# Kernel optimization log

Hardware: AMD Instinct MI355X
Metric: run time of the kernel (lower is better)

## Reference

```python
import jax, jax.numpy as jnp
import numpy as np

NEG_INF = 1e9  # matches module's -1000000000.0 masking constant


def setup_inputs() -> dict:
    key = jax.random.key(0)
    kq, kv = jax.random.split(key)
    B, T, D = 4, 2048, 1024
    query = jax.random.normal(kq, (B, T, D), dtype=jnp.float32)
    value = jax.random.normal(kv, (B, T, D), dtype=jnp.float32)
    return {"query": query, "value": value}


def reference(query, value):
    # key defaults to value (len(inputs) == 2 path)
    k = value
    # dot-product scores (canonical Keras Attention _calculate_scores)
    scores = jnp.einsum("bqd,bkd->bqk", query, k)  # [B, Tq, Tv]
    Tq, Tv = scores.shape[-2], scores.shape[-1]
    # causal lower-triangular mask over last two dims (row >= col)
    causal_mask = jnp.tril(jnp.ones((Tq, Tv), dtype=bool))  # [Tq, Tv]
    # scores -= 1e9 * (~mask), then softmax (eval mode: no dropout)
    scores = scores - NEG_INF * (~causal_mask).astype(scores.dtype)
    weights = jax.nn.softmax(scores, axis=-1)
    result = jnp.einsum("bqv,bvd->bqd", weights, value)
    return result
```

## Files before the change

kernel.cpp:

```cpp
#include <hip/hip_runtime.h>
#include <hip/hip_fp16.h>

typedef _Float16 half8 __attribute__((ext_vector_type(8)));
typedef float    floatx4 __attribute__((ext_vector_type(4)));
typedef unsigned int uintx4 __attribute__((ext_vector_type(4)));

#define MFMA16(a, b, c) __builtin_amdgcn_mfma_f32_16x16x32_f16((a), (b), (c), 0, 0, 0)

constexpr int T_ = 2048;
constexpr int D_ = 1024;
constexpr int NB = 4;
constexpr int NTILE = 136;
constexpr size_t PT_ELEMS = 16384;

__device__ __forceinline__ half8 cvt8(floatx4 a, floatx4 b) {
  half8 h;
  h[0] = (_Float16)a[0]; h[1] = (_Float16)a[1]; h[2] = (_Float16)a[2]; h[3] = (_Float16)a[3];
  h[4] = (_Float16)b[0]; h[5] = (_Float16)b[1]; h[6] = (_Float16)b[2]; h[7] = (_Float16)b[3];
  return h;
}

__device__ __forceinline__ void gl16(const void* g, void* l) {
  __builtin_amdgcn_global_load_lds(
      (const __attribute__((address_space(1))) void*)g,
      (__attribute__((address_space(3))) void*)l, 16, 0, 0);
}

__global__ __launch_bounds__(256) void cast_h(const float* __restrict__ X,
                                              _Float16* __restrict__ Xh) {
  const size_t i = ((size_t)blockIdx.x * 256 + threadIdx.x) * 8;
  *(half8*)(Xh + i) = cvt8(*(const floatx4*)(X + i), *(const floatx4*)(X + i + 4));
}

__global__ __launch_bounds__(256) void build_vt(const float* __restrict__ V,
                                                _Float16* __restrict__ VhT) {
  __shared__ _Float16 tile[64][65];
  const int bid = blockIdx.x;
  const int b = bid & 3, tt = (bid >> 2) & 31, dd = bid >> 7;
  const float* Vb = V + ((size_t)b * T_ + tt * 64) * D_ + dd * 64;
#pragma unroll
  for (int k = 0; k < 16; ++k) {
    const int e = k * 256 + threadIdx.x, r = e >> 6, c = e & 63;
    tile[r][c] = (_Float16)Vb[(size_t)r * D_ + c];
  }
  __syncthreads();
#pragma unroll
  for (int k = 0; k < 16; ++k) {
    const int e = k * 256 + threadIdx.x, dr = e >> 6, tc = e & 63;
    VhT[((size_t)b * D_ + dd * 64 + dr) * T_ + tt * 64 + tc] = tile[tc][dr];
  }
}

__global__ __launch_bounds__(256, 2) void sgemm(const _Float16* __restrict__ Qh,
                                                const _Float16* __restrict__ Vh,
                                                _Float16* __restrict__ Pt,
                                                float* __restrict__ mg,
                                                float* __restrict__ lg) {
  extern __shared__ __align__(16) char lds[];
  char* As = lds;
  char* Bs = lds + 32768;
  const int tid = threadIdx.x;
  const int w = tid >> 6, l = tid & 63, l15 = l & 15, hi = l >> 4;
  const int wr = (w >> 1) * 64, wc = (w & 1) * 64;

  const int b = (int)(blockIdx.x & 3);
  int rem = (int)(blockIdx.x >> 2), j = 0;
  while (rem >= 16 - j) { rem -= 16 - j; ++j; }
  const int i = j + rem;

  const _Float16* Qb = Qh + ((size_t)(b * T_ + i * 128)) * D_;
  const _Float16* Vb = Vh + ((size_t)(b * T_ + j * 128)) * D_;
  const int srow = w * 32 + (l >> 4);
  char* Adst = As + w * 8192;
  char* Bdst = Bs + w * 8192;

  floatx4 acc[4][4];
#pragma unroll
  for (int mi = 0; mi < 4; ++mi)
#pragma unroll
    for (int ni = 0; ni < 4; ++ni) acc[mi][ni] = (floatx4){0.f, 0.f, 0.f, 0.f};

  for (int s = 0; s < 8; ++s) {
#pragma unroll
    for (int q = 0; q < 8; ++q) {
      const int r0 = srow + q * 4;
      const int sc = ((l & 15) ^ (r0 & 15)) * 8;
      gl16(Qb + (size_t)r0 * D_ + s * 128 + sc, Adst + q * 1024);
      gl16(Vb + (size_t)r0 * D_ + s * 128 + sc, Bdst + q * 1024);
    }
    __syncthreads();
#pragma unroll
    for (int s32 = 0; s32 < 4; ++s32) {
      half8 af[4], bb[4];
#pragma unroll
      for (int mi = 0; mi < 4; ++mi) {
        const int row = wr + mi * 16 + l15;
        af[mi] = *(const half8*)(As + row * 256 + (((s32 * 4 + hi) ^ (row & 15)) << 4));
      }
#pragma unroll
      for (int ni = 0; ni < 4; ++ni) {
        const int row = wc + ni * 16 + l15;
        bb[ni] = *(const half8*)(Bs + row * 256 + (((s32 * 4 + hi) ^ (row & 15)) << 4));
      }
#pragma unroll
      for (int mi = 0; mi < 4; ++mi)
#pragma unroll
        for (int ni = 0; ni < 4; ++ni)
          acc[mi][ni] = MFMA16(af[mi], bb[ni], acc[mi][ni]);
    }
    __syncthreads();
  }

  float* Mex = (float*)Bs;
  float* Lex = (float*)(Bs + 1024);

  if (i == j) {
#pragma unroll
    for (int mi = 0; mi < 4; ++mi)
#pragma unroll
      for (int ni = 0; ni < 4; ++ni) {
        const int col = wc + ni * 16 + l15;
        const int row0 = wr + mi * 16 + 4 * hi;
#pragma unroll
        for (int r = 0; r < 4; ++r)
          if (col > row0 + r) acc[mi][ni][r] = -1e30f;
      }
  }

  floatx4 mrow[4];
#pragma unroll
  for (int mi = 0; mi < 4; ++mi) {
#pragma unroll
    for (int r = 0; r < 4; ++r)
      mrow[mi][r] = fmaxf(fmaxf(acc[mi][0][r], acc[mi][1][r]),
                          fmaxf(acc[mi][2][r], acc[mi][3][r]));
#pragma unroll
    for (int off = 1; off < 16; off <<= 1)
#pragma unroll
      for (int r = 0; r < 4; ++r)
        mrow[mi][r] = fmaxf(mrow[mi][r], __shfl_xor(mrow[mi][r], off));
  }
  if (l15 == 0) {
#pragma unroll
    for (int mi = 0; mi < 4; ++mi)
      *(floatx4*)&Mex[(w & 1) * 128 + wr + mi * 16 + 4 * hi] = mrow[mi];
  }
  __syncthreads();
#pragma unroll
  for (int mi = 0; mi < 4; ++mi) {
    const floatx4 m0 = *(const floatx4*)&Mex[wr + mi * 16 + 4 * hi];
    const floatx4 m1 = *(const floatx4*)&Mex[128 + wr + mi * 16 + 4 * hi];
#pragma unroll
    for (int r = 0; r < 4; ++r) mrow[mi][r] = fmaxf(m0[r], m1[r]);
  }

  floatx4 lsum[4];
#pragma unroll
  for (int mi = 0; mi < 4; ++mi) {
    lsum[mi] = (floatx4){0.f, 0.f, 0.f, 0.f};
    const int row0 = wr + mi * 16 + 4 * hi;
#pragma unroll
    for (int ni = 0; ni < 4; ++ni) {
      const int col = wc + ni * 16 + l15;
#pragma unroll
      for (int r = 0; r < 4; ++r) {
        const float p = __expf(acc[mi][ni][r] - mrow[mi][r]);
        lsum[mi][r] += p;
        *(_Float16*)(As + (row0 + r) * 256 + col * 2) = (_Float16)p;
      }
    }
#pragma unroll
    for (int off = 1; off < 16; off <<= 1)
#pragma unroll
      for (int r = 0; r < 4; ++r) lsum[mi][r] += __shfl_xor(lsum[mi][r], off);
  }
  if (l15 == 0) {
#pragma unroll
    for (int mi = 0; mi < 4; ++mi)
      *(floatx4*)&Lex[(w & 1) * 128 + wr + mi * 16 + 4 * hi] = lsum[mi];
  }
  __syncthreads();

  if (((w & 1) == 0) && l15 == 0) {
    const size_t base = ((size_t)(b * 16 + j)) * 2048 + i * 128;
#pragma unroll
    for (int mi = 0; mi < 4; ++mi) {
      const int r0 = wr + mi * 16 + 4 * hi;
      const floatx4 l0 = *(const floatx4*)&Lex[r0];
      const floatx4 l1 = *(const floatx4*)&Lex[128 + r0];
#pragma unroll
      for (int r = 0; r < 4; ++r) {
        mg[base + r0 + r] = mrow[mi][r];
        lg[base + r0 + r] = l0[r] + l1[r];
      }
    }
  }
  _Float16* Pg = Pt + (size_t)(b * NTILE + ((i * (i + 1)) >> 1) + j) * PT_ELEMS;
  const int drow = tid >> 1, dhalf = tid & 1;
#pragma unroll
  for (int k = 0; k < 8; ++k) {
    const int c = k ^ (tid & 7);
    const uintx4 v = *(const uintx4*)(As + drow * 256 + dhalf * 128 + c * 16);
    *(uintx4*)((char*)Pg + drow * 256 + dhalf * 128 + c * 16) = v;
  }
}

__global__ __launch_bounds__(256) void combine(const float* __restrict__ mg,
                                               const float* __restrict__ lg,
                                               _Float16* __restrict__ ah,
                                               float* __restrict__ linv) {
  const int gid = (int)(blockIdx.x * 256 + threadIdx.x);
  const int b = gid >> 11, row = gid & 2047, i = row >> 7;
  const size_t mb = (size_t)b * 32768 + row;
  float M = -1e30f;
  for (int j = 0; j <= i; ++j) M = fmaxf(M, mg[mb + (size_t)j * 2048]);
  float L = 0.f;
  for (int j = 0; j <= i; ++j) {
    const float a = __expf(mg[mb + (size_t)j * 2048] - M);
    L += a * lg[mb + (size_t)j * 2048];
    ah[((size_t)b * 2048 + row) * 16 + j] = (_Float16)a;
  }
  linv[b * 2048 + row] = 1.0f / L;
}

__global__ __launch_bounds__(256, 2) void pv(const _Float16* __restrict__ Pt,
                                             const _Float16* __restrict__ VhT,
                                             const _Float16* __restrict__ ah,
                                             const float* __restrict__ linv,
                                             float* __restrict__ O) {
  extern __shared__ __align__(16) char lds[];
  char* As = lds;
  char* Bs = lds + 32768;
  const int tid = threadIdx.x;
  const int w = tid >> 6, l = tid & 63, l15 = l & 15, hi = l >> 4;
  const int wr = (w >> 1) * 64, wc = (w & 1) * 64;

  const int b = (int)(blockIdx.x & 3), t = (int)(blockIdx.x >> 2);
  const int r_ = t >> 3;
  const int i = (r_ < 8) ? (15 - r_) : (r_ - 8);
  const int nc = t & 7;
  const int ns = i + 1;

  const _Float16* Pb = Pt + (size_t)(b * NTILE + ((i * (i + 1)) >> 1)) * PT_ELEMS;
  const _Float16* Vt = VhT + ((size_t)(b * D_ + nc * 128)) * T_;
  const int srow = w * 32 + (l >> 4);
  char* Adst = As + w * 8192;
  char* Bdst = Bs + w * 8192;

  floatx4 acc[4][4];
#pragma unroll
  for (int mi = 0; mi < 4; ++mi)
#pragma unroll
    for (int ni = 0; ni < 4; ++ni) acc[mi][ni] = (floatx4){0.f, 0.f, 0.f, 0.f};

  for (int s = 0; s < ns; ++s) {
    _Float16 aw[4];
#pragma unroll
    for (int mi = 0; mi < 4; ++mi)
      aw[mi] = ah[((size_t)(b * 2048 + i * 128 + wr + mi * 16 + l15)) * 16 + s];
#pragma unroll
    for (int q = 0; q < 8; ++q) {
      const int r0 = srow + q * 4;
      const int sc = ((l & 15) ^ (r0 & 15)) * 8;
      gl16(Pb + (size_t)s * PT_ELEMS + (size_t)r0 * 128 + sc, Adst + q * 1024);
      gl16(Vt + (size_t)r0 * T_ + s * 128 + sc, Bdst + q * 1024);
    }
    __syncthreads();
#pragma unroll
    for (int s32 = 0; s32 < 4; ++s32) {
      half8 af[4], bb[4];
#pragma unroll
      for (int mi = 0; mi < 4; ++mi) {
        const int row = wr + mi * 16 + l15;
        af[mi] = *(const half8*)(As + row * 256 + (((s32 * 4 + hi) ^ (row & 15)) << 4));
        af[mi] *= aw[mi];
      }
#pragma unroll
      for (int ni = 0; ni < 4; ++ni) {
        const int row = wc + ni * 16 + l15;
        bb[ni] = *(const half8*)(Bs + row * 256 + (((s32 * 4 + hi) ^ (row & 15)) << 4));
      }
#pragma unroll
      for (int mi = 0; mi < 4; ++mi)
#pragma unroll
        for (int ni = 0; ni < 4; ++ni)
          acc[mi][ni] = MFMA16(af[mi], bb[ni], acc[mi][ni]);
    }
    __syncthreads();
  }

  float* Ob = O + ((size_t)b * T_ + i * 128) * D_ + nc * 128;
#pragma unroll
  for (int mi = 0; mi < 4; ++mi)
#pragma unroll
    for (int r = 0; r < 4; ++r) {
      const int rl = wr + mi * 16 + 4 * hi + r;
      const float iv = linv[b * 2048 + i * 128 + rl];
#pragma unroll
      for (int ni = 0; ni < 4; ++ni)
        Ob[(size_t)rl * D_ + wc + ni * 16 + l15] = acc[mi][ni][r] * iv;
    }
}

__global__ __launch_bounds__(256) void attn_fb(const float* __restrict__ Q,
                                               const float* __restrict__ V,
                                               float* __restrict__ O) {
  __shared__ float sc[2048];
  __shared__ float red[4];
  const int b = (int)(blockIdx.x >> 11), m = (int)(blockIdx.x & 2047);
  const int tid = threadIdx.x;
  const float* Qr = Q + ((size_t)b * T_ + m) * D_;
  for (int kv = tid; kv <= m; kv += 256) {
    const float* Vr = V + ((size_t)b * T_ + kv) * D_;
    float s = 0.f;
    for (int d = 0; d < D_; d += 4) {
      floatx4 q4 = *(const floatx4*)(Qr + d), v4 = *(const floatx4*)(Vr + d);
      s += q4[0] * v4[0] + q4[1] * v4[1] + q4[2] * v4[2] + q4[3] * v4[3];
    }
    sc[kv] = s;
  }
  __syncthreads();
  float mx = -1e30f;
  for (int kv = tid; kv <= m; kv += 256) mx = fmaxf(mx, sc[kv]);
#pragma unroll
  for (int off = 1; off < 64; off <<= 1) mx = fmaxf(mx, __shfl_xor(mx, off));
  if ((tid & 63) == 0) red[tid >> 6] = mx;
  __syncthreads();
  mx = fmaxf(fmaxf(red[0], red[1]), fmaxf(red[2], red[3]));
  __syncthreads();
  float sum = 0.f;
  for (int kv = tid; kv <= m; kv += 256) { float p = __expf(sc[kv] - mx); sc[kv] = p; sum += p; }
#pragma unroll
  for (int off = 1; off < 64; off <<= 1) sum += __shfl_xor(sum, off);
  __syncthreads();
  if ((tid & 63) == 0) red[tid >> 6] = sum;
  __syncthreads();
  const float inv = 1.0f / (red[0] + red[1] + red[2] + red[3]);
  float* Or = O + ((size_t)b * T_ + m) * D_;
  const int d = tid * 4;
  floatx4 o = {0.f, 0.f, 0.f, 0.f};
  for (int kv = 0; kv <= m; ++kv) {
    const float p = sc[kv];
    const floatx4 v4 = *(const floatx4*)(V + ((size_t)b * T_ + kv) * D_ + d);
    o[0] += p * v4[0]; o[1] += p * v4[1]; o[2] += p * v4[2]; o[3] += p * v4[3];
  }
  o[0] *= inv; o[1] *= inv; o[2] *= inv; o[3] *= inv;
  *(floatx4*)(Or + d) = o;
}

extern "C" void kernel_launch(void* const* d_in, const int* in_sizes, int n_in,
                              void* d_out, int out_size, void* d_ws, size_t ws_size,
                              hipStream_t stream) {
  const float* q = (const float*)d_in[0];
  const float* v = (const float*)d_in[1];
  float* out = (float*)d_out;

  const size_t OFF_VH = 16777216;
  const size_t OFF_P  = 33554432;
  const size_t OFF_M  = OFF_P + (size_t)NB * NTILE * PT_ELEMS * 2;
  const size_t OFF_LT = OFF_M + 524288;
  const size_t OFF_AH = OFF_LT + 524288;
  const size_t OFF_LI = OFF_AH + 262144;
  const size_t NEED   = OFF_LI + 32768;

  if (ws_size >= NEED) {
    _Float16* qh = (_Float16*)d_ws;
    _Float16* vh = (_Float16*)((char*)d_ws + OFF_VH);
    _Float16* pt = (_Float16*)((char*)d_ws + OFF_P);
    float* mg = (float*)((char*)d_ws + OFF_M);
    float* lg = (float*)((char*)d_ws + OFF_LT);
    _Float16* ah = (_Float16*)((char*)d_ws + OFF_AH);
    float* li = (float*)((char*)d_ws + OFF_LI);
    hipFuncSetAttribute((const void*)sgemm, hipFuncAttributeMaxDynamicSharedMemorySize, 65536);
    hipFuncSetAttribute((const void*)pv, hipFuncAttributeMaxDynamicSharedMemorySize, 65536);
    cast_h<<<dim3(4096), dim3(256), 0, stream>>>(q, qh);
    cast_h<<<dim3(4096), dim3(256), 0, stream>>>(v, vh);
    sgemm<<<dim3(NB * NTILE), dim3(256), 65536, stream>>>(qh, vh, pt, mg, lg);
    combine<<<dim3(32), dim3(256), 0, stream>>>(mg, lg, ah, li);
    build_vt<<<dim3(2048), dim3(256), 0, stream>>>(v, qh);
    pv<<<dim3(512), dim3(256), 65536, stream>>>(pt, qh, ah, li, out);
  } else {
    attn_fb<<<dim3(NB * T_), dim3(256), 0, stream>>>(q, v, out);
  }
}
```

Baseline: 118.2 us.

## Restructure attention pipeline: fused prep, double-buffered 512-thread score and PV GEMMs

Merges the Q cast and V transpose into one prep kernel and drops the separate V fp16 cast: the score GEMM now reads fp32 V straight into LDS and converts it while loading fragments. Both GEMMs move to 512-thread blocks covering 256-row tiles, with double-buffered LDS staging (prefetch the next K slice before the MFMAs) and an explicit waitcnt/barrier sync. PV uses narrower 64-column output tiles, giving more blocks per CU, and zero-fills masked P tiles. This aims to cut launch count, global traffic and load stalls, at the cost of larger LDS use, fp32 B-tile bandwidth and wasted work on partially masked 256-row tiles.

```diff
diff --git a/kernel.cpp b/kernel.cpp
--- a/kernel.cpp
+++ b/kernel.cpp
@@ -11,7 +11,6 @@
 constexpr int D_ = 1024;
 constexpr int NB = 4;
 constexpr int NTILE = 136;
-constexpr size_t PT_ELEMS = 16384;
 
 __device__ __forceinline__ half8 cvt8(floatx4 a, floatx4 b) {
   half8 h;
@@ -26,17 +25,26 @@
       (__attribute__((address_space(3))) void*)l, 16, 0, 0);
 }
 
-__global__ __launch_bounds__(256) void cast_h(const float* __restrict__ X,
-                                              _Float16* __restrict__ Xh) {
-  const size_t i = ((size_t)blockIdx.x * 256 + threadIdx.x) * 8;
-  *(half8*)(Xh + i) = cvt8(*(const floatx4*)(X + i), *(const floatx4*)(X + i + 4));
-}
-
-__global__ __launch_bounds__(256) void build_vt(const float* __restrict__ V,
-                                                _Float16* __restrict__ VhT) {
+__device__ __forceinline__ void STEP_SYNC() {
+  asm volatile("s_waitcnt vmcnt(0) lgkmcnt(0)" ::: "memory");
+  __builtin_amdgcn_s_barrier();
+  __builtin_amdgcn_sched_barrier(0);
+}
+
+__global__ __launch_bounds__(256) void prep(const float* __restrict__ Q,
+                                            const float* __restrict__ V,
+                                            _Float16* __restrict__ Qh,
+                                            _Float16* __restrict__ VhT) {
   __shared__ _Float16 tile[64][65];
   const int bid = blockIdx.x;
-  const int b = bid & 3, tt = (bid >> 2) & 31, dd = bid >> 7;
+  if (bid < 2048) {
+    const size_t i = ((size_t)bid * 256 + threadIdx.x) * 16;
+    *(half8*)(Qh + i)     = cvt8(*(const floatx4*)(Q + i),     *(const floatx4*)(Q + i + 4));
+    *(half8*)(Qh + i + 8) = cvt8(*(const floatx4*)(Q + i + 8), *(const floatx4*)(Q + i + 12));
+    return;
+  }
+  const int b2 = bid - 2048;
+  const int b = b2 & 3, tt = (b2 >> 2) & 31, dd = b2 >> 7;
   const float* Vb = V + ((size_t)b * T_ + tt * 64) * D_ + dd * 64;
 #pragma unroll
   for (int k = 0; k < 16; ++k) {
@@ -51,28 +59,38 @@
   }
 }
 
-__global__ __launch_bounds__(256, 2) void sgemm(const _Float16* __restrict__ Qh,
-                                                const _Float16* __restrict__ Vh,
+__global__ __launch_bounds__(512, 2) void sgemm(const _Float16* __restrict__ Qh,
+                                                const float* __restrict__ V,
                                                 _Float16* __restrict__ Pt,
                                                 float* __restrict__ mg,
                                                 float* __restrict__ lg) {
   extern __shared__ __align__(16) char lds[];
-  char* As = lds;
-  char* Bs = lds + 32768;
   const int tid = threadIdx.x;
   const int w = tid >> 6, l = tid & 63, l15 = l & 15, hi = l >> 4;
   const int wr = (w >> 1) * 64, wc = (w & 1) * 64;
 
   const int b = (int)(blockIdx.x & 3);
   int rem = (int)(blockIdx.x >> 2), j = 0;
-  while (rem >= 16 - j) { rem -= 16 - j; ++j; }
-  const int i = j + rem;
-
-  const _Float16* Qb = Qh + ((size_t)(b * T_ + i * 128)) * D_;
-  const _Float16* Vb = Vh + ((size_t)(b * T_ + j * 128)) * D_;
-  const int srow = w * 32 + (l >> 4);
-  char* Adst = As + w * 8192;
-  char* Bdst = Bs + w * 8192;
+  while (rem >= 8 - (j >> 1)) { rem -= 8 - (j >> 1); ++j; }
+  const int I = (j >> 1) + rem;
+
+  const _Float16* Qb = Qh + ((size_t)(b * T_ + I * 256)) * D_;
+  const float*    Vb = V  + ((size_t)(b * T_ + j * 128)) * D_;
+
+  const int arow = w * 32 + (l >> 3);
+  const int brow = w * 16 + (l >> 4);
+
+  auto STAGE = [&](const int s, const int buf) {
+    char* Ad = lds + buf * 65536 + w * 4096;
+    char* Bd = lds + buf * 65536 + 32768 + w * 4096;
+#pragma unroll
+    for (int q = 0; q < 4; ++q) {
+      const int ar = arow + q * 8;
+      gl16(Qb + (size_t)ar * D_ + s * 64 + ((l & 7) ^ (ar & 7)) * 8, Ad + q * 1024);
+      const int br = brow + q * 4;
+      gl16(Vb + (size_t)br * D_ + s * 64 + ((l & 15) ^ (br & 15)) * 4, Bd + q * 1024);
+    }
+  };
 
   floatx4 acc[4][4];
 #pragma unroll
@@ -80,53 +98,66 @@
 #pragma unroll
     for (int ni = 0; ni < 4; ++ni) acc[mi][ni] = (floatx4){0.f, 0.f, 0.f, 0.f};
 
-  for (int s = 0; s < 8; ++s) {
-#pragma unroll
-    for (int q = 0; q < 8; ++q) {
-      const int r0 = srow + q * 4;
-      const int sc = ((l & 15) ^ (r0 & 15)) * 8;
-      gl16(Qb + (size_t)r0 * D_ + s * 128 + sc, Adst + q * 1024);
-      gl16(Vb + (size_t)r0 * D_ + s * 128 + sc, Bdst + q * 1024);
-    }
-    __syncthreads();
-#pragma unroll
-    for (int s32 = 0; s32 < 4; ++s32) {
-      half8 af[4], bb[4];
-#pragma unroll
-      for (int mi = 0; mi < 4; ++mi) {
-        const int row = wr + mi * 16 + l15;
-        af[mi] = *(const half8*)(As + row * 256 + (((s32 * 4 + hi) ^ (row & 15)) << 4));
-      }
-#pragma unroll
-      for (int ni = 0; ni < 4; ++ni) {
-        const int row = wc + ni * 16 + l15;
-        bb[ni] = *(const half8*)(Bs + row * 256 + (((s32 * 4 + hi) ^ (row & 15)) << 4));
-      }
-#pragma unroll
-      for (int mi = 0; mi < 4; ++mi)
-#pragma unroll
-        for (int ni = 0; ni < 4; ++ni)
-          acc[mi][ni] = MFMA16(af[mi], bb[ni], acc[mi][ni]);
-    }
-    __syncthreads();
-  }
-
-  float* Mex = (float*)Bs;
-  float* Lex = (float*)(Bs + 1024);
-
-  if (i == j) {
-#pragma unroll
-    for (int mi = 0; mi < 4; ++mi)
-#pragma unroll
-      for (int ni = 0; ni < 4; ++ni) {
-        const int col = wc + ni * 16 + l15;
-        const int row0 = wr + mi * 16 + 4 * hi;
-#pragma unroll
-        for (int r = 0; r < 4; ++r)
-          if (col > row0 + r) acc[mi][ni][r] = -1e30f;
-      }
-  }
-
+  STAGE(0, 0);
+  STEP_SYNC();
+  for (int s = 0; s < 16; ++s) {
+    const int cur = s & 1;
+    const char* Ab = lds + cur * 65536;
+    const char* Bb = lds + cur * 65536 + 32768;
+    half8 af[4], bb[4];
+#pragma unroll
+    for (int mi = 0; mi < 4; ++mi) {
+      const int row = wr + mi * 16 + l15;
+      af[mi] = *(const half8*)(Ab + row * 128 + ((hi ^ (row & 7)) << 4));
+    }
+#pragma unroll
+    for (int ni = 0; ni < 4; ++ni) {
+      const int row = wc + ni * 16 + l15;
+      const int p = (hi * 2) ^ (row & 15);
+      const floatx4 f0 = *(const floatx4*)(Bb + row * 256 + (p << 4));
+      const floatx4 f1 = *(const floatx4*)(Bb + row * 256 + ((p << 4) ^ 16));
+      bb[ni] = cvt8(f0, f1);
+    }
+    if (s + 1 < 16) STAGE(s + 1, cur ^ 1);
+#pragma unroll
+    for (int mi = 0; mi < 4; ++mi)
+#pragma unroll
+      for (int ni = 0; ni < 4; ++ni)
+        acc[mi][ni] = MFMA16(af[mi], bb[ni], acc[mi][ni]);
+#pragma unroll
+    for (int mi = 0; mi < 4; ++mi) {
+      const int row = wr + mi * 16 + l15;
+      af[mi] = *(const half8*)(Ab + row * 128 + (((4 + hi) ^ (row & 7)) << 4));
+    }
+#pragma unroll
+    for (int ni = 0; ni < 4; ++ni) {
+      const int row = wc + ni * 16 + l15;
+      const int p = (8 + hi * 2) ^ (row & 15);
+      const floatx4 f0 = *(const floatx4*)(Bb + row * 256 + (p << 4));
+      const floatx4 f1 = *(const floatx4*)(Bb + row * 256 + ((p << 4) ^ 16));
+      bb[ni] = cvt8(f0, f1);
+    }
+#pragma unroll
+    for (int mi = 0; mi < 4; ++mi)
+#pragma unroll
+      for (int ni = 0; ni < 4; ++ni)
+        acc[mi][ni] = MFMA16(af[mi], bb[ni], acc[mi][ni]);
+    STEP_SYNC();
+  }
+
+  float* Mex = (float*)lds;
+  float* Lex = (float*)(lds + 2048);
+#pragma unroll
+  for (int mi = 0; mi < 4; ++mi) {
+    const int row0 = I * 256 + wr + mi * 16 + 4 * hi;
+#pragma unroll
+    for (int ni = 0; ni < 4; ++ni) {
+      const int col = j * 128 + wc + ni * 16 + l15;
+#pragma unroll
+      for (int r = 0; r < 4; ++r)
+        if (col > row0 + r) acc[mi][ni][r] = -1e30f;
+    }
+  }
   floatx4 mrow[4];
 #pragma unroll
   for (int mi = 0; mi < 4; ++mi) {
@@ -143,65 +174,74 @@
   if (l15 == 0) {
 #pragma unroll
     for (int mi = 0; mi < 4; ++mi)
-      *(floatx4*)&Mex[(w & 1) * 128 + wr + mi * 16 + 4 * hi] = mrow[mi];
+      *(floatx4*)&Mex[(w & 1) * 256 + wr + mi * 16 + 4 * hi] = mrow[mi];
   }
   __syncthreads();
 #pragma unroll
   for (int mi = 0; mi < 4; ++mi) {
-    const floatx4 m0 = *(const floatx4*)&Mex[wr + mi * 16 + 4 * hi];
-    const floatx4 m1 = *(const floatx4*)&Mex[128 + wr + mi * 16 + 4 * hi];
+    const int r0 = wr + mi * 16 + 4 * hi;
+    const floatx4 m0 = *(const floatx4*)&Mex[r0];
+    const floatx4 m1 = *(const floatx4*)&Mex[256 + r0];
 #pragma unroll
     for (int r = 0; r < 4; ++r) mrow[mi][r] = fmaxf(m0[r], m1[r]);
   }
-
-  floatx4 lsum[4];
+  char* Pw = (w >> 2) ? (lds + 98304) : (lds + 65536);
+  floatx4 ls[4];
 #pragma unroll
   for (int mi = 0; mi < 4; ++mi) {
-    lsum[mi] = (floatx4){0.f, 0.f, 0.f, 0.f};
-    const int row0 = wr + mi * 16 + 4 * hi;
+    ls[mi] = (floatx4){0.f, 0.f, 0.f, 0.f};
+    const int rl = (wr & 127) + mi * 16 + 4 * hi;
 #pragma unroll
     for (int ni = 0; ni < 4; ++ni) {
       const int col = wc + ni * 16 + l15;
 #pragma unroll
       for (int r = 0; r < 4; ++r) {
         const float p = __expf(acc[mi][ni][r] - mrow[mi][r]);
-        lsum[mi][r] += p;
-        *(_Float16*)(As + (row0 + r) * 256 + col * 2) = (_Float16)p;
+        ls[mi][r] += p;
+        *(_Float16*)(Pw + (rl + r) * 256 + col * 2) = (_Float16)p;
       }
     }
 #pragma unroll
     for (int off = 1; off < 16; off <<= 1)
 #pragma unroll
-      for (int r = 0; r < 4; ++r) lsum[mi][r] += __shfl_xor(lsum[mi][r], off);
+      for (int r = 0; r < 4; ++r) ls[mi][r] += __shfl_xor(ls[mi][r], off);
   }
   if (l15 == 0) {
 #pragma unroll
     for (int mi = 0; mi < 4; ++mi)
-      *(floatx4*)&Lex[(w & 1) * 128 + wr + mi * 16 + 4 * hi] = lsum[mi];
+      *(floatx4*)&Lex[(w & 1) * 256 + wr + mi * 16 + 4 * hi] = ls[mi];
   }
   __syncthreads();
 
   if (((w & 1) == 0) && l15 == 0) {
-    const size_t base = ((size_t)(b * 16 + j)) * 2048 + i * 128;
+    const size_t base = ((size_t)(b * 16 + j)) * 2048;
 #pragma unroll
     for (int mi = 0; mi < 4; ++mi) {
       const int r0 = wr + mi * 16 + 4 * hi;
-      const floatx4 l0 = *(const floatx4*)&Lex[r0];
-      const floatx4 l1 = *(const floatx4*)&Lex[128 + r0];
-#pragma unroll
-      for (int r = 0; r < 4; ++r) {
-        mg[base + r0 + r] = mrow[mi][r];
-        lg[base + r0 + r] = l0[r] + l1[r];
+      const int gr = I * 256 + r0;
+      if (gr >= j * 128) {
+#pragma unroll
+        for (int r = 0; r < 4; ++r) {
+          mg[base + gr + r] = mrow[mi][r];
+          lg[base + gr + r] = Lex[r0 + r] + Lex[256 + r0 + r];
+        }
       }
     }
   }
-  _Float16* Pg = Pt + (size_t)(b * NTILE + ((i * (i + 1)) >> 1) + j) * PT_ELEMS;
-  const int drow = tid >> 1, dhalf = tid & 1;
-#pragma unroll
-  for (int k = 0; k < 8; ++k) {
-    const int c = k ^ (tid & 7);
-    const uintx4 v = *(const uintx4*)(As + drow * 256 + dhalf * 128 + c * 16);
-    *(uintx4*)((char*)Pg + drow * 256 + dhalf * 128 + c * 16) = v;
+  {
+    const int th = tid >> 8, tt = tid & 255;
+    const int it = 2 * I + th;
+    if (j <= it) {
+      char* Pg = (char*)(Pt + ((size_t)(b * NTILE + ((it * (it + 1)) >> 1) + j)) * 16384);
+      const char* src = th ? (lds + 98304) : (lds + 65536);
+      const int drow = tt >> 1, dh = tt & 1;
+#pragma unroll
+      for (int k = 0; k < 8; ++k) {
+        const int c = k ^ (tt & 7);
+        *(uintx4*)(Pg + drow * 256 + dh * 128 + c * 16) =
+            *(const uintx4*)(src + drow * 256 + dh * 128 + c * 16);
+      }
+    }
   }
 }
 
@@ -223,81 +263,112 @@
   linv[b * 2048 + row] = 1.0f / L;
 }
 
-__global__ __launch_bounds__(256, 2) void pv(const _Float16* __restrict__ Pt,
+__global__ __launch_bounds__(512, 4) void pv(const _Float16* __restrict__ Pt,
                                              const _Float16* __restrict__ VhT,
                                              const _Float16* __restrict__ ah,
                                              const float* __restrict__ linv,
                                              float* __restrict__ O) {
   extern __shared__ __align__(16) char lds[];
-  char* As = lds;
-  char* Bs = lds + 32768;
   const int tid = threadIdx.x;
   const int w = tid >> 6, l = tid & 63, l15 = l & 15, hi = l >> 4;
-  const int wr = (w >> 1) * 64, wc = (w & 1) * 64;
-
-  const int b = (int)(blockIdx.x & 3), t = (int)(blockIdx.x >> 2);
-  const int r_ = t >> 3;
-  const int i = (r_ < 8) ? (15 - r_) : (r_ - 8);
-  const int nc = t & 7;
-  const int ns = i + 1;
-
-  const _Float16* Pb = Pt + (size_t)(b * NTILE + ((i * (i + 1)) >> 1)) * PT_ELEMS;
-  const _Float16* Vt = VhT + ((size_t)(b * D_ + nc * 128)) * T_;
-  const int srow = w * 32 + (l >> 4);
-  char* Adst = As + w * 8192;
-  char* Bdst = Bs + w * 8192;
-
-  floatx4 acc[4][4];
+  const int wr = (w >> 1) * 64, wc = (w & 1) * 32;
+
+  const int b = (int)(blockIdx.x & 3);
+  const int u = (int)(blockIdx.x >> 2);
+  const int r_ = u >> 4;
+  const int I = (r_ < 4) ? (7 - r_) : (r_ - 4);
+  const int nc = u & 15;
+  const int ns = 4 * I + 4;
+
+  const int h = w >> 2;
+  const int it = 2 * I + h;
+  const int arow = w * 32 + (l >> 3);
+  const int vrow = w * 8 + (l >> 3);
+
+  auto STAGE = [&](const int s, const int buf) {
+    char* Ad = lds + buf * 40960 + w * 4096;
+    char* Bd = lds + buf * 40960 + 32768 + w * 1024;
+    const int jt = s >> 1;
+    if (jt <= it) {
+      const _Float16* Pb = Pt + ((size_t)(b * NTILE + ((it * (it + 1)) >> 1) + jt)) * 16384;
+#pragma unroll
+      for (int q = 0; q < 4; ++q) {
+        const int ar = arow + q * 8;
+        gl16(Pb + (size_t)(ar & 127) * 128 + (s & 1) * 64 + ((l & 7) ^ (ar & 7)) * 8,
+             Ad + q * 1024);
+      }
+    } else {
+#pragma unroll
+      for (int q = 0; q < 4; ++q)
+        *(uintx4*)(Ad + q * 1024 + l * 16) = (uintx4){0u, 0u, 0u, 0u};
+    }
+    gl16(VhT + ((size_t)(b * D_ + nc * 64 + vrow)) * T_ + s * 64 + ((l & 7) ^ (vrow & 7)) * 8,
+         Bd);
+  };
+
+  floatx4 acc[4][2];
 #pragma unroll
   for (int mi = 0; mi < 4; ++mi)
 #pragma unroll
-    for (int ni = 0; ni < 4; ++ni) acc[mi][ni] = (floatx4){0.f, 0.f, 0.f, 0.f};
-
+    for (int ni = 0; ni < 2; ++ni) acc[mi][ni] = (floatx4){0.f, 0.f, 0.f, 0.f};
+
+  STAGE(0, 0);
+  STEP_SYNC();
   for (int s = 0; s < ns; ++s) {
+    const int cur = s & 1;
+    const char* Ab = lds + cur * 40960;
+    const char* Bb = lds + cur * 40960 + 32768;
+    const int jt = s >> 1;
     _Float16 aw[4];
 #pragma unroll
     for (int mi = 0; mi < 4; ++mi)
-      aw[mi] = ah[((size_t)(b * 2048 + i * 128 + wr + mi * 16 + l15)) * 16 + s];
-#pragma unroll
-    for (int q = 0; q < 8; ++q) {
-      const int r0 = srow + q * 4;
-      const int sc = ((l & 15) ^ (r0 & 15)) * 8;
-      gl16(Pb + (size_t)s * PT_ELEMS + (size_t)r0 * 128 + sc, Adst + q * 1024);
-      gl16(Vt + (size_t)r0 * T_ + s * 128 + sc, Bdst + q * 1024);
-    }
-    __syncthreads();
-#pragma unroll
-    for (int s32 = 0; s32 < 4; ++s32) {
-      half8 af[4], bb[4];
-#pragma unroll
-      for (int mi = 0; mi < 4; ++mi) {
-        const int row = wr + mi * 16 + l15;
-        af[mi] = *(const half8*)(As + row * 256 + (((s32 * 4 + hi) ^ (row & 15)) << 4));
-        af[mi] *= aw[mi];
-      }
-#pragma unroll
-      for (int ni = 0; ni < 4; ++ni) {
-        const int row = wc + ni * 16 + l15;
-        bb[ni] = *(const half8*)(Bs + row * 256 + (((s32 * 4 + hi) ^ (row & 15)) << 4));
-      }
-#pragma unroll
-      for (int mi = 0; mi < 4; ++mi)
-#pragma unroll
-        for (int ni = 0; ni < 4; ++ni)
-          acc[mi][ni] = MFMA16(af[mi], bb[ni], acc[mi][ni]);
-    }
-    __syncthreads();
-  }
-
-  float* Ob = O + ((size_t)b * T_ + i * 128) * D_ + nc * 128;
+      aw[mi] = ah[((size_t)(b * T_ + I * 256 + wr + mi * 16 + l15)) * 16 + jt];
+    half8 af[4], bb[2];
+#pragma unroll
+    for (int mi = 0; mi < 4; ++mi) {
+      const int row = wr + mi * 16 + l15;
+      af[mi] = *(const half8*)(Ab + row * 128 + ((hi ^ (row & 7)) << 4));
+      af[mi] *= aw[mi];
+    }
+#pragma unroll
+    for (int ni = 0; ni < 2; ++ni) {
+      const int row = wc + ni * 16 + l15;
+      bb[ni] = *(const half8*)(Bb + row * 128 + ((hi ^ (row & 7)) << 4));
+    }
+    if (s + 1 < ns) STAGE(s + 1, cur ^ 1);
+#pragma unroll
+    for (int mi = 0; mi < 4; ++mi)
+#pragma unroll
+      for (int ni = 0; ni < 2; ++ni)
+        acc[mi][ni] = MFMA16(af[mi], bb[ni], acc[mi][ni]);
+#pragma unroll
+    for (int mi = 0; mi < 4; ++mi) {
+      const int row = wr + mi * 16 + l15;
+      af[mi] = *(const half8*)(Ab + row * 128 + (((4 + hi) ^ (row & 7)) << 4));
+      af[mi] *= aw[mi];
+    }
+#pragma unroll
+    for (int ni = 0; ni < 2; ++ni) {
+      const int row = wc + ni * 16 + l15;
+      bb[ni] = *(const half8*)(Bb + row * 128 + (((4 + hi) ^ (row & 7)) << 4));
+    }
+#pragma unroll
+    for (int mi = 0; mi < 4; ++mi)
+#pragma unroll
+      for (int ni = 0; ni < 2; ++ni)
+        acc[mi][ni] = MFMA16(af[mi], bb[ni], acc[mi][ni]);
+    STEP_SYNC();
+  }
+
+  float* Ob = O + ((size_t)(b * T_ + I * 256)) * D_ + nc * 64;
 #pragma unroll
   for (int mi = 0; mi < 4; ++mi)
 #pragma unroll
     for (int r = 0; r < 4; ++r) {
       const int rl = wr + mi * 16 + 4 * hi + r;
-      const float iv = linv[b * 2048 + i * 128 + rl];
-#pragma unroll
-      for (int ni = 0; ni < 4; ++ni)
+      const float iv = linv[b * T_ + I * 256 + rl];
+#pragma unroll
+      for (int ni = 0; ni < 2; ++ni)
         Ob[(size_t)rl * D_ + wc + ni * 16 + l15] = acc[mi][ni][r] * iv;
     }
 }
@@ -355,30 +426,28 @@
   const float* v = (const float*)d_in[1];
   float* out = (float*)d_out;
 
-  const size_t OFF_VH = 16777216;
+  const size_t OFF_VT = 16777216;
   const size_t OFF_P  = 33554432;
-  const size_t OFF_M  = OFF_P + (size_t)NB * NTILE * PT_ELEMS * 2;
-  const size_t OFF_LT = OFF_M + 524288;
-  const size_t OFF_AH = OFF_LT + 524288;
+  const size_t OFF_M  = OFF_P + (size_t)NB * NTILE * 16384 * 2;
+  const size_t OFF_LG = OFF_M + 524288;
+  const size_t OFF_AH = OFF_LG + 524288;
   const size_t OFF_LI = OFF_AH + 262144;
   const size_t NEED   = OFF_LI + 32768;
 
   if (ws_size >= NEED) {
     _Float16* qh = (_Float16*)d_ws;
-    _Float16* vh = (_Float16*)((char*)d_ws + OFF_VH);
+    _Float16* vt = (_Float16*)((char*)d_ws + OFF_VT);
     _Float16* pt = (_Float16*)((char*)d_ws + OFF_P);
     float* mg = (float*)((char*)d_ws + OFF_M);
-    float* lg = (float*)((char*)d_ws + OFF_LT);
+    float* lg = (float*)((char*)d_ws + OFF_LG);
     _Float16* ah = (_Float16*)((char*)d_ws + OFF_AH);
     float* li = (float*)((char*)d_ws + OFF_LI);
-    hipFuncSetAttribute((const void*)sgemm, hipFuncAttributeMaxDynamicSharedMemorySize, 65536);
-    hipFuncSetAttribute((const void*)pv, hipFuncAttributeMaxDynamicSharedMemorySize, 65536);
-    cast_h<<<dim3(4096), dim3(256), 0, stream>>>(q, qh);
-    cast_h<<<dim3(4096), dim3(256), 0, stream>>>(v, vh);
-    sgemm<<<dim3(NB * NTILE), dim3(256), 65536, stream>>>(qh, vh, pt, mg, lg);
+    hipFuncSetAttribute((const void*)sgemm, hipFuncAttributeMaxDynamicSharedMemorySize, 131072);
+    hipFuncSetAttribute((const void*)pv, hipFuncAttributeMaxDynamicSharedMemorySize, 81920);
+    prep<<<dim3(4096), dim3(256), 0, stream>>>(q, v, qh, vt);
+    sgemm<<<dim3(NB * 72), dim3(512), 131072, stream>>>(qh, v, pt, mg, lg);
     combine<<<dim3(32), dim3(256), 0, stream>>>(mg, lg, ah, li);
-    build_vt<<<dim3(2048), dim3(256), 0, stream>>>(v, qh);
-    pv<<<dim3(512), dim3(256), 65536, stream>>>(pt, qh, ah, li, out);
+    pv<<<dim3(512), dim3(512), 81920, stream>>>(pt, vt, ah, li, out);
   } else {
     attn_fb<<<dim3(NB * T_), dim3(256), 0, stream>>>(q, v, out);
   }
```

New measurement: 145.9 us. 1.23x slower.
